# Kernel optimization log

Measured on AMD Instinct MI355X. Metric: run time of the kernel, lower is better.

Reference implementation:

```python
import jax, jax.numpy as jnp
import numpy as np

H, W = 1024, 1024        # heatmap resolution
C = 128                  # n_targets (clusters)
N_ITER = 8               # n_iterations


def setup_inputs() -> dict:
    key = jax.random.key(0)
    k1, k2 = jax.random.split(key)
    # clusters live in pixel coordinate space [0,H) x [0,W)
    clusters = jax.random.uniform(k1, (C, 2), dtype=jnp.float32) * jnp.array([H, W], dtype=jnp.float32)
    heatmap = jax.random.uniform(k2, (H, W), dtype=jnp.float32)
    return {"clusters": clusters, "heatmap": heatmap}


def reference(clusters, heatmap):
    # pixel coordinate grid [H, W, 2] with (row, col) ordering, matching
    # clusters[c,0]-row, clusters[c,1]-col in the original code
    rows = jnp.arange(H, dtype=jnp.float32)
    cols = jnp.arange(W, dtype=jnp.float32)
    coords = jnp.stack(jnp.meshgrid(rows, cols, indexing='ij'), axis=-1)  # [H, W, 2]

    def step(cs, _):
        # Euclidean distance from every pixel to every cluster, clamped to >= 1
        diff = coords[:, :, None, :] - cs[None, None, :, :]          # [H, W, C, 2]
        dist = jnp.maximum(1.0, jnp.sqrt(jnp.sum(diff * diff, axis=-1)))  # [H, W, C]
        assign = jnp.argmin(dist, axis=-1)                            # [H, W] nearest cluster
        best_dist = jnp.min(dist, axis=-1)                            # [H, W]
        # weighted scatter-add of pixel coords into their nearest cluster
        contrib = coords * (heatmap / best_dist)[..., None]           # [H, W, 2]
        new_cs = jax.ops.segment_sum(contrib.reshape(-1, 2), assign.reshape(-1), num_segments=C)
        return new_cs.astype(jnp.float32), None

    cs, _ = jax.lax.scan(step, clusters, None, length=N_ITER)
    return cs
```

## Files before the change

kernel.cpp:

```cpp
#include <hip/hip_runtime.h>
#include <float.h>

constexpr int H = 1024, W = 1024, C = 128, N_ITER = 8;
constexpr int TPB = 256;
constexpr int TILE = 32;
constexpr int PPT = 4;
constexpr int K = 32;
constexpr int SLOTS = 2 * C;
constexpr int NBLK = (H / TILE) * (W / TILE);
constexpr int NCNT = 128;
constexpr int CNT_STRIDE = 16;
constexpr int ARRIVE_DEPTH = NBLK / NCNT;
constexpr int NREP = 16;
constexpr unsigned SIGNB = 0x80000000u;

__device__ __forceinline__ void waitVmem() {
    asm volatile("s_waitcnt vmcnt(0)" ::: "memory");
}

__global__ __launch_bounds__(TPB, 4) void kmeans_fused(
    const float* __restrict__ cur0,
    const float* __restrict__ heatmap,
    float* __restrict__ shards,
    int*   __restrict__ barCnt,
    unsigned* __restrict__ clsPub,
    float* __restrict__ out)
{
    __shared__ float2 cls[C];
    __shared__ float2 cand[C];
    __shared__ int    candIdx[C];
    __shared__ float  waveMin[2];
    __shared__ int    waveCnt[2];
    __shared__ float  acc[SLOTS];
    __shared__ unsigned char dupf[C];

    const int tid = threadIdx.x;
    const int bid = blockIdx.x;

    if (bid == 0) {
        for (int it = 0; it < N_ITER; ++it) {
            if (tid < NCNT) {
                int* cptr = barCnt + ((size_t)it * NCNT + tid) * CNT_STRIDE;
                while (__hip_atomic_load(cptr, __ATOMIC_RELAXED,
                                         __HIP_MEMORY_SCOPE_AGENT) < ARRIVE_DEPTH)
                    __builtin_amdgcn_s_sleep(1);
            }
            __syncthreads();

            const float* b = shards + (size_t)it * K * SLOTS + tid;
            float v[K];
#pragma unroll
            for (int k = 0; k < K; ++k)
                v[k] = __hip_atomic_load(b + (size_t)k * SLOTS,
                                         __ATOMIC_RELAXED, __HIP_MEMORY_SCOPE_AGENT);
            float s = 0.0f;
#pragma unroll
            for (int k = 0; k < K; ++k) s += v[k];

            if (it == N_ITER - 1) {
                out[tid] = s;
                return;
            }

            if (tid < C) dupf[tid] = 0;
            ((float*)cls)[tid] = s;
            __syncthreads();
            {
                const int    sdi  = tid & (C - 1);
                const float2 sdme = cls[sdi];
                const int kLo = (tid < C) ? 1 : 33;
#pragma unroll 8
                for (int kk = 0; kk < 32; ++kk) {
                    const int k = kLo + kk;
                    const int j = (sdi + k) & (C - 1);
                    const float2 o = cls[j];
                    if (o.x == sdme.x && o.y == sdme.y)
                        dupf[(sdi + k < C) ? (sdi + k) : sdi] = 1;
                }
            }
            __syncthreads();

            const float pv = dupf[tid >> 1] ? (float)INFINITY : s;
            const unsigned enc = __float_as_uint(pv) ^ SIGNB;
            unsigned* pb = clsPub + (size_t)it * NREP * SLOTS;
#pragma unroll
            for (int r = 0; r < NREP; ++r)
                __hip_atomic_store(pb + r * SLOTS + tid, enc,
                                   __ATOMIC_RELAXED, __HIP_MEMORY_SCOPE_AGENT);
        }
        return;
    }

    const int wid   = bid - 1;
    const int tileR = (wid >> 5) * TILE;
    const int tileC = (wid & 31) * TILE;

    const int   rowIn = tid >> 3;
    const float fr    = (float)(tileR + rowIn);
    const int   col0  = tileC + (tid & 7) * PPT;
    const float4 h4   = *(const float4*)(heatmap + (size_t)(tileR + rowIn) * W + col0);
    float hval[PPT] = { h4.x, h4.y, h4.z, h4.w };
    float colf[PPT];
#pragma unroll
    for (int p = 0; p < PPT; ++p) colf[p] = (float)(col0 + p);

    for (int it = 0; it < N_ITER; ++it) {
        float coord;
        if (it == 0) {
            coord = cur0[tid];
        } else {
            const unsigned* src = clsPub
                + ((size_t)(it - 1) * NREP + (wid & (NREP - 1))) * SLOTS;
            unsigned u;
            for (;;) {
                u = __hip_atomic_load(src + tid, __ATOMIC_RELAXED,
                                      __HIP_MEMORY_SCOPE_AGENT);
                if (__ballot(u != 0u) == 0xFFFFFFFFFFFFFFFFull) break;
                __builtin_amdgcn_s_sleep(4);
            }
            coord = __uint_as_float(u ^ SIGNB);
        }

        acc[tid] = 0.0f;
        ((float*)cls)[tid] = coord;
        __syncthreads();

        float dcen = 0.0f;
        if (tid < C) {
            const float2 cl = cls[tid];
            const float dxr = cl.x - ((float)tileR + 15.5f);
            const float dyc = cl.y - ((float)tileC + 15.5f);
            dcen = sqrtf(dxr * dxr + dyc * dyc);
            float m = dcen;
#pragma unroll
            for (int off = 32; off > 0; off >>= 1)
                m = fminf(m, __shfl_xor(m, off));
            if ((tid & 63) == 0) waveMin[tid >> 6] = m;
        }
        __syncthreads();

        bool keep = false;
        int  pre  = 0;
        if (tid < C) {
            const float thr = fminf(waveMin[0], waveMin[1]) + 44.84062f;
            keep = (dcen <= thr);
            const unsigned long long mask = __ballot(keep);
            const int lane = tid & 63;
            pre = __popcll(mask & ((1ull << lane) - 1ull));
            if (lane == 0) waveCnt[tid >> 6] = __popcll(mask);
        }
        __syncthreads();
        if (keep) {
            const int pos = pre + ((tid >= 64) ? waveCnt[0] : 0);
            cand[pos]    = cls[tid];
            candIdx[pos] = tid;
        }
        __syncthreads();

        const int nCand = waveCnt[0] + waveCnt[1];

        float best[PPT];
        int   bi[PPT];
#pragma unroll
        for (int p = 0; p < PPT; ++p) { best[p] = FLT_MAX; bi[p] = 0; }

        for (int k = 0; k < nCand; ++k) {
            const float2 cl = cand[k];
            const int    ci = candIdx[k];
            const float  dx  = fr - cl.x;
            const float  dx2 = dx * dx;
#pragma unroll
            for (int p = 0; p < PPT; ++p) {
                const float dy  = colf[p] - cl.y;
                const float d2  = fmaf(dy, dy, dx2);
                const float key = fmaxf(d2, 1.0f);
                const bool  lt  = key < best[p];
                bi[p]   = lt ? ci  : bi[p];
                best[p] = lt ? key : best[p];
            }
        }

#pragma unroll
        for (int p = 0; p < PPT; ++p) {
            const float bd  = fmaxf(1.0f, sqrtf(best[p]));
            const float wgt = hval[p] / bd;
            float v0 = fr      * wgt;
            float v1 = colf[p] * wgt;
            const int b0 = __shfl(bi[p], 0);
            if (__ballot(bi[p] == b0) == 0xFFFFFFFFFFFFFFFFull) {
#pragma unroll
                for (int off = 32; off > 0; off >>= 1) {
                    v0 += __shfl_xor(v0, off);
                    v1 += __shfl_xor(v1, off);
                }
                if ((tid & 63) == 0) {
                    unsafeAtomicAdd(&acc[2 * b0 + 0], v0);
                    unsafeAtomicAdd(&acc[2 * b0 + 1], v1);
                }
            } else {
                unsafeAtomicAdd(&acc[2 * bi[p] + 0], v0);
                unsafeAtomicAdd(&acc[2 * bi[p] + 1], v1);
            }
        }
        __syncthreads();

        const float a = acc[tid];
        if (a != 0.0f)
            unsafeAtomicAdd(&shards[(size_t)it * K * SLOTS
                                    + (wid & (K - 1)) * SLOTS + tid], a);

        waitVmem();
        __syncthreads();
        if (tid == 0)
            __hip_atomic_fetch_add(
                barCnt + ((size_t)it * NCNT + (wid & (NCNT - 1))) * CNT_STRIDE, 1,
                __ATOMIC_RELAXED, __HIP_MEMORY_SCOPE_AGENT);
    }
}

extern "C" void kernel_launch(void* const* d_in, const int* in_sizes, int n_in,
                              void* d_out, int out_size, void* d_ws, size_t ws_size,
                              hipStream_t stream) {
    const float* clusters = (const float*)d_in[0];
    const float* heatmap  = (const float*)d_in[1];
    float* out = (float*)d_out;

    float* shards = (float*)d_ws;
    const size_t shardBytes = (size_t)N_ITER * K * SLOTS * sizeof(float);
    int* barCnt = (int*)((char*)d_ws + shardBytes);
    const size_t cntBytes = (size_t)N_ITER * NCNT * CNT_STRIDE * sizeof(int);
    unsigned* clsPub = (unsigned*)((char*)barCnt + cntBytes);
    const size_t pubBytes = (size_t)N_ITER * NREP * SLOTS * sizeof(unsigned);

    hipMemsetAsync(d_ws, 0, shardBytes + cntBytes + pubBytes, stream);

    kmeans_fused<<<NBLK + 1, TPB, 0, stream>>>(clusters, heatmap, shards,
                                               barCnt, clsPub, out);
}
```

Before: 141.7 us.

## Zero next-iteration workspace in-kernel and poll published clusters with wide uncached loads

The workspace is reorganised into per-iteration slices. The host memset now clears only the first slice, and each worker block zeroes its share of the next slice during the current iteration, which shrinks the memset before launch. Polling for published clusters now uses one wave issuing four cache-bypassing loads per lane with a shorter sleep, instead of every thread spinning on one load. This relies on the in-kernel zeroing being ordered before anyone reads the next slice, which the per-iteration barrier has to guarantee.

```diff
diff --git a/kernel.cpp b/kernel.cpp
--- a/kernel.cpp
+++ b/kernel.cpp
@@ -14,19 +14,33 @@
 constexpr int NREP = 16;
 constexpr unsigned SIGNB = 0x80000000u;
 
+constexpr int SHARD_WORDS = K * SLOTS;
+constexpr int CNT_WORDS   = NCNT * CNT_STRIDE;
+constexpr int PUB_WORDS   = NREP * SLOTS;
+constexpr int SLICE_WORDS = SHARD_WORDS + CNT_WORDS + PUB_WORDS;
+constexpr int ZERO_PER_BLK = SLICE_WORDS / NBLK;
+
 __device__ __forceinline__ void waitVmem() {
     asm volatile("s_waitcnt vmcnt(0)" ::: "memory");
+}
+
+__device__ __forceinline__ float* sliceShards(unsigned* ws, int it) {
+    return (float*)(ws + (size_t)it * SLICE_WORDS);
+}
+__device__ __forceinline__ int* sliceCnt(unsigned* ws, int it) {
+    return (int*)(ws + (size_t)it * SLICE_WORDS + SHARD_WORDS);
+}
+__device__ __forceinline__ unsigned* slicePub(unsigned* ws, int it) {
+    return ws + (size_t)it * SLICE_WORDS + SHARD_WORDS + CNT_WORDS;
 }
 
 __global__ __launch_bounds__(TPB, 4) void kmeans_fused(
     const float* __restrict__ cur0,
     const float* __restrict__ heatmap,
-    float* __restrict__ shards,
-    int*   __restrict__ barCnt,
-    unsigned* __restrict__ clsPub,
+    unsigned* __restrict__ ws,
     float* __restrict__ out)
 {
-    __shared__ float2 cls[C];
+    __shared__ __align__(16) float2 cls[C];
     __shared__ float2 cand[C];
     __shared__ int    candIdx[C];
     __shared__ float  waveMin[2];
@@ -39,15 +53,16 @@
 
     if (bid == 0) {
         for (int it = 0; it < N_ITER; ++it) {
-            if (tid < NCNT) {
-                int* cptr = barCnt + ((size_t)it * NCNT + tid) * CNT_STRIDE;
+            {
+                int* cptr = sliceCnt(ws, it) + (tid & (NCNT - 1)) * CNT_STRIDE;
+                if (tid >= NCNT) __builtin_amdgcn_s_sleep(1);
                 while (__hip_atomic_load(cptr, __ATOMIC_RELAXED,
                                          __HIP_MEMORY_SCOPE_AGENT) < ARRIVE_DEPTH)
                     __builtin_amdgcn_s_sleep(1);
             }
             __syncthreads();
 
-            const float* b = shards + (size_t)it * K * SLOTS + tid;
+            const float* b = sliceShards(ws, it) + tid;
             float v[K];
 #pragma unroll
             for (int k = 0; k < K; ++k)
@@ -82,7 +97,7 @@
 
             const float pv = dupf[tid >> 1] ? (float)INFINITY : s;
             const unsigned enc = __float_as_uint(pv) ^ SIGNB;
-            unsigned* pb = clsPub + (size_t)it * NREP * SLOTS;
+            unsigned* pb = slicePub(ws, it);
 #pragma unroll
             for (int r = 0; r < NREP; ++r)
                 __hip_atomic_store(pb + r * SLOTS + tid, enc,
@@ -105,24 +120,33 @@
     for (int p = 0; p < PPT; ++p) colf[p] = (float)(col0 + p);
 
     for (int it = 0; it < N_ITER; ++it) {
-        float coord;
+        acc[tid] = 0.0f;
         if (it == 0) {
-            coord = cur0[tid];
-        } else {
-            const unsigned* src = clsPub
-                + ((size_t)(it - 1) * NREP + (wid & (NREP - 1))) * SLOTS;
-            unsigned u;
+            ((float*)cls)[tid] = cur0[tid];
+        } else if (tid < 64) {
+            const unsigned* src = slicePub(ws, it - 1)
+                + (wid & (NREP - 1)) * SLOTS + tid * 4;
+            unsigned a0, a1, a2, a3;
             for (;;) {
-                u = __hip_atomic_load(src + tid, __ATOMIC_RELAXED,
-                                      __HIP_MEMORY_SCOPE_AGENT);
-                if (__ballot(u != 0u) == 0xFFFFFFFFFFFFFFFFull) break;
-                __builtin_amdgcn_s_sleep(4);
-            }
-            coord = __uint_as_float(u ^ SIGNB);
-        }
-
-        acc[tid] = 0.0f;
-        ((float*)cls)[tid] = coord;
+                asm volatile(
+                    "global_load_dword %0, %4, off sc0 sc1\n\t"
+                    "global_load_dword %1, %5, off sc0 sc1\n\t"
+                    "global_load_dword %2, %6, off sc0 sc1\n\t"
+                    "global_load_dword %3, %7, off sc0 sc1\n\t"
+                    "s_waitcnt vmcnt(0)"
+                    : "=&v"(a0), "=&v"(a1), "=&v"(a2), "=&v"(a3)
+                    : "v"(src), "v"(src + 1), "v"(src + 2), "v"(src + 3)
+                    : "memory");
+                const bool ok = (a0 != 0u) & (a1 != 0u) & (a2 != 0u) & (a3 != 0u);
+                if (__ballot(ok) == 0xFFFFFFFFFFFFFFFFull) break;
+                __builtin_amdgcn_s_sleep(1);
+            }
+            float* c4 = (float*)cls + tid * 4;
+            c4[0] = __uint_as_float(a0 ^ SIGNB);
+            c4[1] = __uint_as_float(a1 ^ SIGNB);
+            c4[2] = __uint_as_float(a2 ^ SIGNB);
+            c4[3] = __uint_as_float(a3 ^ SIGNB);
+        }
         __syncthreads();
 
         float dcen = 0.0f;
@@ -206,14 +230,18 @@
 
         const float a = acc[tid];
         if (a != 0.0f)
-            unsafeAtomicAdd(&shards[(size_t)it * K * SLOTS
-                                    + (wid & (K - 1)) * SLOTS + tid], a);
+            unsafeAtomicAdd(sliceShards(ws, it) + (wid & (K - 1)) * SLOTS + tid, a);
+
+        if (it < N_ITER - 1 && tid < ZERO_PER_BLK)
+            __hip_atomic_store(ws + (size_t)(it + 1) * SLICE_WORDS
+                                   + wid * ZERO_PER_BLK + tid,
+                               0u, __ATOMIC_RELAXED, __HIP_MEMORY_SCOPE_AGENT);
 
         waitVmem();
         __syncthreads();
         if (tid == 0)
             __hip_atomic_fetch_add(
-                barCnt + ((size_t)it * NCNT + (wid & (NCNT - 1))) * CNT_STRIDE, 1,
+                sliceCnt(ws, it) + (wid & (NCNT - 1)) * CNT_STRIDE, 1,
                 __ATOMIC_RELAXED, __HIP_MEMORY_SCOPE_AGENT);
     }
 }
@@ -225,15 +253,9 @@
     const float* heatmap  = (const float*)d_in[1];
     float* out = (float*)d_out;
 
-    float* shards = (float*)d_ws;
-    const size_t shardBytes = (size_t)N_ITER * K * SLOTS * sizeof(float);
-    int* barCnt = (int*)((char*)d_ws + shardBytes);
-    const size_t cntBytes = (size_t)N_ITER * NCNT * CNT_STRIDE * sizeof(int);
-    unsigned* clsPub = (unsigned*)((char*)barCnt + cntBytes);
-    const size_t pubBytes = (size_t)N_ITER * NREP * SLOTS * sizeof(unsigned);
-
-    hipMemsetAsync(d_ws, 0, shardBytes + cntBytes + pubBytes, stream);
-
-    kmeans_fused<<<NBLK + 1, TPB, 0, stream>>>(clusters, heatmap, shards,
-                                               barCnt, clsPub, out);
-}
+    unsigned* ws = (unsigned*)d_ws;
+
+    hipMemsetAsync(d_ws, 0, (size_t)SLICE_WORDS * sizeof(unsigned), stream);
+
+    kmeans_fused<<<NBLK + 1, TPB, 0, stream>>>(clusters, heatmap, ws, out);
+}
```

New measurement: 149.0 us. +5.1%, slower.
